# Performance work log

Hardware: AMD Instinct MI355X
Metric: run time of the kernel (lower is better)

## Reference

```python
import jax, jax.numpy as jnp
import numpy as np

ORD = 2  # matches EarthMoverLoss(ord=2)


def _lsa_square(cost):
    """Optimal linear sum assignment (minimize) on a square cost matrix.
    Shortest-augmenting-path algorithm, equivalent to
    scipy.optimize.linear_sum_assignment. Returns col4row: row i -> col4row[i].
    """
    n = cost.shape[0]
    u = np.zeros(n)
    v = np.zeros(n)
    path = np.full(n, -1, dtype=np.int64)
    col4row = np.full(n, -1, dtype=np.int64)
    row4col = np.full(n, -1, dtype=np.int64)
    rows = np.arange(n)
    for cur_row in range(n):
        min_val = 0.0
        i = cur_row
        SR = np.zeros(n, dtype=bool)   # scanned rows
        SC = np.zeros(n, dtype=bool)   # scanned cols
        shortest = np.full(n, np.inf)  # shortest path cost to each col
        sink = -1
        while sink == -1:
            SR[i] = True
            cols = np.flatnonzero(~SC)
            r = min_val + cost[i, cols] - u[i] - v[cols]
            upd = r < shortest[cols]
            cu = cols[upd]
            shortest[cu] = r[upd]
            path[cu] = i
            k = np.argmin(shortest[cols])
            j = cols[k]
            min_val = shortest[j]
            if np.isinf(min_val):
                raise ValueError('infeasible cost matrix')
            SC[j] = True
            if row4col[j] == -1:
                sink = j
            else:
                i = row4col[j]
        # dual variable update
        u[cur_row] += min_val
        others = SR & (rows != cur_row)
        u[others] += min_val - shortest[col4row[others]]
        v[SC] -= min_val - shortest[SC]
        # augment along the alternating path
        j = sink
        while True:
            i = path[j]
            row4col[j] = i
            col4row[i], j = j, col4row[i]
            if i == cur_row:
                break
    return col4row


def _batched_assignment(x, y):
    """Per-sample Euclidean cdist + Hungarian; mirrors the torch module's
    detached CPU/scipy path. Returns [B, N] int permutation of y per sample."""
    xn = np.asarray(jax.device_get(x), dtype=np.float64)
    yn = np.asarray(jax.device_get(y), dtype=np.float64)
    perms = []
    for b in range(xn.shape[0]):
        d2 = ((xn[b, :, None, :] - yn[b, None, :, :]) ** 2).sum(-1)  # [N, N]
        perms.append(_lsa_square(np.sqrt(d2)))
    return jnp.asarray(np.stack(perms))  # [B, N]


def setup_inputs() -> dict:
    key = jax.random.key(0)
    k1, k2 = jax.random.split(key)
    pred = jax.random.normal(k1, (8, 256, 3), dtype=jnp.float32)
    label = jax.random.normal(k2, (8, 256, 3), dtype=jnp.float32)
    return {"pred": pred, "label": label}


def reference(pred, label):
    # Hungarian matching on detached values (scipy returns ind1 = arange for
    # a square cost matrix, so only label is permuted).
    perm = _batched_assignment(pred, label)                      # [B, N]
    matched_y = jnp.take_along_axis(label, perm[:, :, None], axis=1)  # [B, N, D]
    # mean over batch and points of the ord-2 vector norm along coord dim
    return jnp.mean(jnp.linalg.norm(pred - matched_y, ord=ORD, axis=2))
```

## Files before the change

kernel.cpp:

```cpp
#include <hip/hip_runtime.h>
#include <math.h>

#define NPTS 256
#define NB 8

#if __has_builtin(__builtin_amdgcn_sqrtf)
#define FSQRT __builtin_amdgcn_sqrtf
#else
#define FSQRT sqrtf
#endif

__device__ __forceinline__ double dist3d(double ax, double ay, double az,
                                         double bx, double by, double bz) {
#pragma clang fp contract(off)
  double d0 = ax - bx;
  double d1 = ay - by;
  double d2 = az - bz;
  double s = d0 * d0;
  s = s + d1 * d1;
  s = s + d2 * d2;
  return sqrt(s);
}

__device__ __forceinline__ float distf(float ax, float ay, float az,
                                       float bx, float by, float bz) {
  float d0 = ax - bx, d1 = ay - by, d2 = az - bz;
  return FSQRT(d0 * d0 + d1 * d1 + d2 * d2);
}

__device__ __forceinline__ unsigned wave_min_u32(unsigned x) {
  unsigned r = x;
  r = min(r, (unsigned)__builtin_amdgcn_update_dpp((int)r, (int)r, 0x111, 0xF, 0xF, false));
  r = min(r, (unsigned)__builtin_amdgcn_update_dpp((int)r, (int)r, 0x112, 0xF, 0xF, false));
  r = min(r, (unsigned)__builtin_amdgcn_update_dpp((int)r, (int)r, 0x114, 0xF, 0xF, false));
  r = min(r, (unsigned)__builtin_amdgcn_update_dpp((int)r, (int)r, 0x118, 0xF, 0xF, false));
  r = min(r, (unsigned)__builtin_amdgcn_update_dpp((int)r, (int)r, 0x142, 0xF, 0xF, false));
  r = min(r, (unsigned)__builtin_amdgcn_update_dpp((int)r, (int)r, 0x143, 0xF, 0xF, false));
  return (unsigned)__builtin_amdgcn_readlane((int)r, 63);
}

__global__ __launch_bounds__(64) void emd_lsa_kernel(
    const float* __restrict__ pred, const float* __restrict__ label,
    double* __restrict__ partial) {
  __shared__ float4 rowd[NPTS];
  __shared__ float ys0[NPTS], ys1[NPTS], ys2[NPTS];
  __shared__ float short_l[NPTS];
  __shared__ int path_l[NPTS];
  __shared__ int c4r_l[NPTS];
  __shared__ int r4c_l[NPTS];
  __shared__ int sr_l[NPTS];
  __shared__ int bcfr[NPTS];
  __shared__ int fq[NPTS];

  const int lane = threadIdx.x;
  const int b = blockIdx.x;
  const float* xg = pred + (size_t)b * NPTS * 3;
  const float* yg = label + (size_t)b * NPTS * 3;

  const int cid0 = lane * 4, cid1 = cid0 + 1, cid2 = cid0 + 2, cid3 = cid0 + 3;

  float q0x, q0y, q0z, q1x, q1y, q1z, q2x, q2y, q2z, q3x, q3y, q3z;
  float vv0, vv1, vv2, vv3;
  int rc0, rc1, rc2, rc3;

#define INITC(c) { int j = cid##c; \
    rowd[j] = make_float4(xg[j*3+0], xg[j*3+1], xg[j*3+2], 0.0f); \
    float t0 = yg[j*3+0], t1 = yg[j*3+1], t2 = yg[j*3+2]; \
    ys0[j] = t0; ys1[j] = t1; ys2[j] = t2; \
    q##c##x = t0; q##c##y = t1; q##c##z = t2; \
    c4r_l[j] = -1; r4c_l[j] = -1; bcfr[j] = 0x7FFFFFFF; }
  INITC(0) INITC(1) INITC(2) INITC(3)
#undef INITC
  __syncthreads();

  float mm0 = 3.4e38f, mm1 = 3.4e38f, mm2 = 3.4e38f, mm3 = 3.4e38f;
  int im0 = -1, im1 = -1, im2 = -1, im3 = -1;
  for (int i = 0; i < NPTS; ++i) {
    float4 rd = rowd[i];
#define CRED(c) { float d = distf(rd.x, rd.y, rd.z, q##c##x, q##c##y, q##c##z); \
    bool u_ = d < mm##c; mm##c = u_ ? d : mm##c; im##c = u_ ? i : im##c; }
    CRED(0) CRED(1) CRED(2) CRED(3)
#undef CRED
  }
  vv0 = mm0; vv1 = mm1; vv2 = mm2; vv3 = mm3;
  atomicMin(&bcfr[im0], cid0);
  atomicMin(&bcfr[im1], cid1);
  atomicMin(&bcfr[im2], cid2);
  atomicMin(&bcfr[im3], cid3);
  __syncthreads();
  if (bcfr[im0] == cid0) { r4c_l[cid0] = im0; c4r_l[im0] = cid0; }
  if (bcfr[im1] == cid1) { r4c_l[cid1] = im1; c4r_l[im1] = cid1; }
  if (bcfr[im2] == cid2) { r4c_l[cid2] = im2; c4r_l[im2] = cid2; }
  if (bcfr[im3] == cid3) { r4c_l[cid3] = im3; c4r_l[im3] = cid3; }
  __syncthreads();
  rc0 = r4c_l[cid0]; rc1 = r4c_l[cid1]; rc2 = r4c_l[cid2]; rc3 = r4c_l[cid3];

  int nf;
  {
    int4 cc = *(int4*)&c4r_l[cid0];
    bool f0 = cc.x < 0, f1 = cc.y < 0, f2 = cc.z < 0, f3 = cc.w < 0;
    unsigned long long b0 = __ballot(f0), b1 = __ballot(f1);
    unsigned long long b2 = __ballot(f2), b3 = __ballot(f3);
    unsigned long long lt = (1ull << lane) - 1ull;
    int off = __popcll(b0 & lt) + __popcll(b1 & lt) + __popcll(b2 & lt) + __popcll(b3 & lt);
    if (f0) fq[off++] = cid0;
    if (f1) fq[off++] = cid1;
    if (f2) fq[off++] = cid2;
    if (f3) fq[off++] = cid3;
    nf = __popcll(b0) + __popcll(b1) + __popcll(b2) + __popcll(b3);
  }
  __syncthreads();

  const float INF = 3.4e38f;

  for (int t = 0; t < nf; ++t) {
    int cur_row = fq[t];

    float sh0 = INF, sh1 = INF, sh2 = INF, sh3 = INF;
    int pp0 = -1, pp1 = -1, pp2 = -1, pp3 = -1;
    int sc0 = 0, sc1 = 0, sc2 = 0, sc3 = 0;
    *(int4*)&sr_l[cid0] = make_int4(0, 0, 0, 0);
    __syncthreads();

    float min_val = 0.0f;
    int i = cur_row;
    int sink = -1;
    float xi, yi, zi, ui;
    { float4 r0 = rowd[cur_row]; xi = r0.x; yi = r0.y; zi = r0.z; ui = r0.w; }

    while (true) {
      sr_l[i] = 1;
      float base = min_val - ui;
      unsigned k0, k1, k2, k3;
#define SSTEP(c) { float d = distf(xi, yi, zi, q##c##x, q##c##y, q##c##z); \
      float r = (base + d) - vv##c; \
      bool u_ = (r < sh##c) && (sc##c == 0); \
      sh##c = u_ ? r : sh##c; \
      pp##c = u_ ? i : pp##c; \
      unsigned kk = (__float_as_uint(fmaxf(sh##c, 0.0f)) & 0xFFFFFF00u) | (unsigned)cid##c; \
      k##c = sc##c ? 0xFFFFFFFFu : kk; }
      SSTEP(0) SSTEP(1) SSTEP(2) SSTEP(3)
#undef SSTEP
      bool t01 = k1 < k0;
      unsigned ka = t01 ? k1 : k0; int na = t01 ? rc1 : rc0;
      float ea = t01 ? sh1 : sh0;  int pa = t01 ? pp1 : pp0;
      bool t23 = k3 < k2;
      unsigned kb = t23 ? k3 : k2; int nb2 = t23 ? rc3 : rc2;
      float eb = t23 ? sh3 : sh2;  int pb = t23 ? pp3 : pp2;
      bool tf = kb < ka;
      unsigned lkey = tf ? kb : ka; int nl = tf ? nb2 : na;
      float el = tf ? eb : ea;     int pl = tf ? pb : pa;

      float4 pre = rowd[nl < 0 ? 0 : nl];

      unsigned best = wave_min_u32(lkey);
      int jstar = (int)(best & 0xFFu);
      int w = jstar >> 2;

      int nr = __builtin_amdgcn_readlane(nl, w);
      min_val = __int_as_float(__builtin_amdgcn_readlane(__float_as_int(el), w));
      int pj = __builtin_amdgcn_readlane(pl, w);

      short_l[jstar] = min_val;
      path_l[jstar] = pj;
      sc0 |= (cid0 == jstar); sc1 |= (cid1 == jstar);
      sc2 |= (cid2 == jstar); sc3 |= (cid3 == jstar);

      if (nr < 0) { sink = jstar; break; }
      i = nr;
      xi = __int_as_float(__builtin_amdgcn_readlane(__float_as_int(pre.x), w));
      yi = __int_as_float(__builtin_amdgcn_readlane(__float_as_int(pre.y), w));
      zi = __int_as_float(__builtin_amdgcn_readlane(__float_as_int(pre.z), w));
      ui = __int_as_float(__builtin_amdgcn_readlane(__float_as_int(pre.w), w));
    }
    __syncthreads();

#define DUALU(c) { int row = cid##c; \
      if (sr_l[row]) { \
        float du = (row == cur_row) ? min_val : (min_val - short_l[c4r_l[row]]); \
        rowd[row].w += du; } \
      if (sc##c) vv##c -= min_val - sh##c; }
    DUALU(0) DUALU(1) DUALU(2) DUALU(3)
#undef DUALU
    __syncthreads();

    if (lane == 0) {
      int jj = sink;
      while (true) {
        int ii = path_l[jj];
        r4c_l[jj] = ii;
        int tmp = c4r_l[ii];
        c4r_l[ii] = jj;
        jj = tmp;
        if (ii == cur_row) break;
      }
    }
    __syncthreads();
    rc0 = r4c_l[cid0]; rc1 = r4c_l[cid1]; rc2 = r4c_l[cid2]; rc3 = r4c_l[cid3];
    __syncthreads();
  }

  double s = 0.0;
#define FIN(c) { int row = cid##c; int j = c4r_l[row]; float4 rd = rowd[row]; \
    s += dist3d((double)rd.x, (double)rd.y, (double)rd.z, \
                (double)ys0[j], (double)ys1[j], (double)ys2[j]); }
  FIN(0) FIN(1) FIN(2) FIN(3)
#undef FIN
  for (int m = 1; m < 64; m <<= 1) s += __shfl_xor(s, m);
  if (lane == 0) partial[b] = s;
}

__global__ void emd_finalize_kernel(const double* __restrict__ partial,
                                    float* __restrict__ out) {
  if (threadIdx.x == 0 && blockIdx.x == 0) {
    double s = 0.0;
    for (int b = 0; b < NB; ++b) s += partial[b];
    out[0] = (float)(s / (double)(NB * NPTS));
  }
}

extern "C" void kernel_launch(void* const* d_in, const int* in_sizes, int n_in,
                              void* d_out, int out_size, void* d_ws, size_t ws_size,
                              hipStream_t stream) {
  const float* pred = (const float*)d_in[0];
  const float* label = (const float*)d_in[1];
  double* partial = (double*)d_ws;
  emd_lsa_kernel<<<NB, 64, 0, stream>>>(pred, label, partial);
  emd_finalize_kernel<<<1, 64, 0, stream>>>(partial, (float*)d_out);
}
```

Baseline: 1.420 ms.

## Pack two samples per wave and add row-reduction dual initialization

Each 64-lane wave now solves two samples in parallel, one per 32-lane half, with 8 columns per lane. Only 4 blocks are launched instead of 8. A row-reduction pass tightens the dual variables before augmentation, which may shorten the augmenting paths. The per-step cross-lane reduction now uses DPP plus ds_bpermute within each half instead of readlanes, and the wave-wide barriers inside the augment loop are dropped. In exchange each lane does twice the work per step, and both halves run in lockstep until the larger of the two free-row counts is done.

```diff
diff --git a/kernel.cpp b/kernel.cpp
--- a/kernel.cpp
+++ b/kernel.cpp
@@ -10,12 +10,12 @@
 #define FSQRT sqrtf
 #endif
 
+#define REP8(M) M(0) M(1) M(2) M(3) M(4) M(5) M(6) M(7)
+
 __device__ __forceinline__ double dist3d(double ax, double ay, double az,
                                          double bx, double by, double bz) {
 #pragma clang fp contract(off)
-  double d0 = ax - bx;
-  double d1 = ay - by;
-  double d2 = az - bz;
+  double d0 = ax - bx, d1 = ay - by, d2 = az - bz;
   double s = d0 * d0;
   s = s + d1 * d1;
   s = s + d2 * d2;
@@ -28,186 +28,213 @@
   return FSQRT(d0 * d0 + d1 * d1 + d2 * d2);
 }
 
-__device__ __forceinline__ unsigned wave_min_u32(unsigned x) {
+__device__ __forceinline__ unsigned grp_min_bcast(unsigned x, int bad31) {
   unsigned r = x;
   r = min(r, (unsigned)__builtin_amdgcn_update_dpp((int)r, (int)r, 0x111, 0xF, 0xF, false));
   r = min(r, (unsigned)__builtin_amdgcn_update_dpp((int)r, (int)r, 0x112, 0xF, 0xF, false));
   r = min(r, (unsigned)__builtin_amdgcn_update_dpp((int)r, (int)r, 0x114, 0xF, 0xF, false));
   r = min(r, (unsigned)__builtin_amdgcn_update_dpp((int)r, (int)r, 0x118, 0xF, 0xF, false));
   r = min(r, (unsigned)__builtin_amdgcn_update_dpp((int)r, (int)r, 0x142, 0xF, 0xF, false));
-  r = min(r, (unsigned)__builtin_amdgcn_update_dpp((int)r, (int)r, 0x143, 0xF, 0xF, false));
-  return (unsigned)__builtin_amdgcn_readlane((int)r, 63);
-}
+  return (unsigned)__builtin_amdgcn_ds_bpermute(bad31, (int)r);
+}
+
+__device__ __forceinline__ float bperm_f(int ba, float v) {
+  return __int_as_float(__builtin_amdgcn_ds_bpermute(ba, __float_as_int(v)));
+}
+
+#define SEL8(T, res, P, cs) { \
+  T a01 = ((cs) & 1) ? P##1 : P##0; T a23 = ((cs) & 1) ? P##3 : P##2; \
+  T a45 = ((cs) & 1) ? P##5 : P##4; T a67 = ((cs) & 1) ? P##7 : P##6; \
+  T a03 = ((cs) & 2) ? a23 : a01;   T a47 = ((cs) & 2) ? a67 : a45; \
+  res = ((cs) & 4) ? a47 : a03; }
 
 __global__ __launch_bounds__(64) void emd_lsa_kernel(
     const float* __restrict__ pred, const float* __restrict__ label,
     double* __restrict__ partial) {
-  __shared__ float4 rowd[NPTS];
-  __shared__ float ys0[NPTS], ys1[NPTS], ys2[NPTS];
-  __shared__ float short_l[NPTS];
-  __shared__ int path_l[NPTS];
-  __shared__ int c4r_l[NPTS];
-  __shared__ int r4c_l[NPTS];
-  __shared__ int sr_l[NPTS];
-  __shared__ int bcfr[NPTS];
-  __shared__ int fq[NPTS];
+  __shared__ float4 rowd[2 * NPTS];
+  __shared__ float4 colj[2 * NPTS];
+  __shared__ float short_l[2 * NPTS];
+  __shared__ int path_l[2 * NPTS];
+  __shared__ int c4r_l[2 * NPTS];
+  __shared__ int r4c_l[2 * NPTS];
+  __shared__ int sr_l[2 * NPTS];
+  __shared__ int bcfr[2 * NPTS];
+  __shared__ int fq[2 * NPTS];
 
   const int lane = threadIdx.x;
+  const int gid = lane >> 5;
+  const int gl = lane & 31;
+  const int gofs = gid << 8;
   const int b = blockIdx.x;
-  const float* xg = pred + (size_t)b * NPTS * 3;
-  const float* yg = label + (size_t)b * NPTS * 3;
-
-  const int cid0 = lane * 4, cid1 = cid0 + 1, cid2 = cid0 + 2, cid3 = cid0 + 3;
-
-  float q0x, q0y, q0z, q1x, q1y, q1z, q2x, q2y, q2z, q3x, q3y, q3z;
-  float vv0, vv1, vv2, vv3;
-  int rc0, rc1, rc2, rc3;
-
-#define INITC(c) { int j = cid##c; \
-    rowd[j] = make_float4(xg[j*3+0], xg[j*3+1], xg[j*3+2], 0.0f); \
+  const int smp = 2 * b + gid;
+  const float* xg = pred + (size_t)smp * NPTS * 3;
+  const float* yg = label + (size_t)smp * NPTS * 3;
+  const int bad31 = ((lane & 32) | 31) << 2;
+  const int rb = gl << 3;
+
+#define DECL(c) float q##c##x, q##c##y, q##c##z; float vv##c; int rc##c;
+  REP8(DECL)
+#undef DECL
+
+#define INITC(c) { int j = rb + c; int g = gofs + j; \
+    rowd[g] = make_float4(xg[j*3+0], xg[j*3+1], xg[j*3+2], 0.0f); \
     float t0 = yg[j*3+0], t1 = yg[j*3+1], t2 = yg[j*3+2]; \
-    ys0[j] = t0; ys1[j] = t1; ys2[j] = t2; \
+    colj[g] = make_float4(t0, t1, t2, 0.0f); \
     q##c##x = t0; q##c##y = t1; q##c##z = t2; \
-    c4r_l[j] = -1; r4c_l[j] = -1; bcfr[j] = 0x7FFFFFFF; }
-  INITC(0) INITC(1) INITC(2) INITC(3)
+    c4r_l[g] = -1; r4c_l[g] = -1; bcfr[g] = 0x7FFFFFFF; }
+  REP8(INITC)
 #undef INITC
   __syncthreads();
 
-  float mm0 = 3.4e38f, mm1 = 3.4e38f, mm2 = 3.4e38f, mm3 = 3.4e38f;
-  int im0 = -1, im1 = -1, im2 = -1, im3 = -1;
+#define DECLM(c) float mm##c = 3.4e38f; int im##c = -1;
+  REP8(DECLM)
+#undef DECLM
   for (int i = 0; i < NPTS; ++i) {
-    float4 rd = rowd[i];
+    float4 rd = rowd[gofs + i];
 #define CRED(c) { float d = distf(rd.x, rd.y, rd.z, q##c##x, q##c##y, q##c##z); \
     bool u_ = d < mm##c; mm##c = u_ ? d : mm##c; im##c = u_ ? i : im##c; }
-    CRED(0) CRED(1) CRED(2) CRED(3)
+    REP8(CRED)
 #undef CRED
   }
-  vv0 = mm0; vv1 = mm1; vv2 = mm2; vv3 = mm3;
-  atomicMin(&bcfr[im0], cid0);
-  atomicMin(&bcfr[im1], cid1);
-  atomicMin(&bcfr[im2], cid2);
-  atomicMin(&bcfr[im3], cid3);
-  __syncthreads();
-  if (bcfr[im0] == cid0) { r4c_l[cid0] = im0; c4r_l[im0] = cid0; }
-  if (bcfr[im1] == cid1) { r4c_l[cid1] = im1; c4r_l[im1] = cid1; }
-  if (bcfr[im2] == cid2) { r4c_l[cid2] = im2; c4r_l[im2] = cid2; }
-  if (bcfr[im3] == cid3) { r4c_l[cid3] = im3; c4r_l[im3] = cid3; }
-  __syncthreads();
-  rc0 = r4c_l[cid0]; rc1 = r4c_l[cid1]; rc2 = r4c_l[cid2]; rc3 = r4c_l[cid3];
+#define WRV(c) colj[gofs + rb + c].w = mm##c; atomicMin(&bcfr[gofs + im##c], rb + c);
+  REP8(WRV)
+#undef WRV
+  __syncthreads();
+#define GRD(c) if (bcfr[gofs + im##c] == rb + c) { r4c_l[gofs + rb + c] = im##c; c4r_l[gofs + im##c] = rb + c; }
+  REP8(GRD)
+#undef GRD
+  __syncthreads();
+
+  {
+#define LDR(c) float4 rD##c = rowd[gofs + rb + c]; int ja##c = c4r_l[gofs + rb + c]; float mu##c = 3.4e38f;
+    REP8(LDR)
+#undef LDR
+    for (int j = 0; j < NPTS; ++j) {
+      float4 cj = colj[gofs + j];
+#define RT(c) { float d = distf(rD##c.x, rD##c.y, rD##c.z, cj.x, cj.y, cj.z) - cj.w; \
+      d = (j == ja##c) ? 3.4e38f : d; mu##c = fminf(mu##c, d); }
+      REP8(RT)
+#undef RT
+    }
+#define WRT(c) if (ja##c >= 0) { colj[gofs + ja##c].w -= mu##c; rowd[gofs + rb + c].w = mu##c; }
+    REP8(WRT)
+#undef WRT
+  }
+  __syncthreads();
+#define LDV(c) vv##c = colj[gofs + rb + c].w; rc##c = r4c_l[gofs + rb + c];
+  REP8(LDV)
+#undef LDV
 
   int nf;
   {
-    int4 cc = *(int4*)&c4r_l[cid0];
-    bool f0 = cc.x < 0, f1 = cc.y < 0, f2 = cc.z < 0, f3 = cc.w < 0;
-    unsigned long long b0 = __ballot(f0), b1 = __ballot(f1);
-    unsigned long long b2 = __ballot(f2), b3 = __ballot(f3);
-    unsigned long long lt = (1ull << lane) - 1ull;
-    int off = __popcll(b0 & lt) + __popcll(b1 & lt) + __popcll(b2 & lt) + __popcll(b3 & lt);
-    if (f0) fq[off++] = cid0;
-    if (f1) fq[off++] = cid1;
-    if (f2) fq[off++] = cid2;
-    if (f3) fq[off++] = cid3;
-    nf = __popcll(b0) + __popcll(b1) + __popcll(b2) + __popcll(b3);
-  }
-  __syncthreads();
+#define FLG(c) int fl##c = (c4r_l[gofs + rb + c] < 0) ? 1 : 0; \
+    unsigned long long bb##c = __ballot(fl##c); \
+    unsigned gm##c = (unsigned)(bb##c >> (gid * 32));
+    REP8(FLG)
+#undef FLG
+    unsigned lt = (1u << gl) - 1u;
+    int off = __popc(gm0 & lt) + __popc(gm1 & lt) + __popc(gm2 & lt) + __popc(gm3 & lt)
+            + __popc(gm4 & lt) + __popc(gm5 & lt) + __popc(gm6 & lt) + __popc(gm7 & lt);
+#define PUT(c) if (fl##c) { fq[gofs + off] = rb + c; off++; }
+    REP8(PUT)
+#undef PUT
+    nf = __popc(gm0) + __popc(gm1) + __popc(gm2) + __popc(gm3)
+       + __popc(gm4) + __popc(gm5) + __popc(gm6) + __popc(gm7);
+  }
+  __syncthreads();
+  int onf = __shfl(nf, lane ^ 32);
+  int nfmax = max(nf, onf);
 
   const float INF = 3.4e38f;
 
-  for (int t = 0; t < nf; ++t) {
-    int cur_row = fq[t];
-
-    float sh0 = INF, sh1 = INF, sh2 = INF, sh3 = INF;
-    int pp0 = -1, pp1 = -1, pp2 = -1, pp3 = -1;
-    int sc0 = 0, sc1 = 0, sc2 = 0, sc3 = 0;
-    *(int4*)&sr_l[cid0] = make_int4(0, 0, 0, 0);
-    __syncthreads();
-
-    float min_val = 0.0f;
-    int i = cur_row;
-    int sink = -1;
-    float xi, yi, zi, ui;
-    { float4 r0 = rowd[cur_row]; xi = r0.x; yi = r0.y; zi = r0.z; ui = r0.w; }
-
-    while (true) {
-      sr_l[i] = 1;
-      float base = min_val - ui;
-      unsigned k0, k1, k2, k3;
-#define SSTEP(c) { float d = distf(xi, yi, zi, q##c##x, q##c##y, q##c##z); \
-      float r = (base + d) - vv##c; \
-      bool u_ = (r < sh##c) && (sc##c == 0); \
-      sh##c = u_ ? r : sh##c; \
-      pp##c = u_ ? i : pp##c; \
-      unsigned kk = (__float_as_uint(fmaxf(sh##c, 0.0f)) & 0xFFFFFF00u) | (unsigned)cid##c; \
-      k##c = sc##c ? 0xFFFFFFFFu : kk; }
-      SSTEP(0) SSTEP(1) SSTEP(2) SSTEP(3)
+  for (int t = 0; t < nfmax; ++t) {
+    bool act = (t < nf);
+    if (act) {
+      int cur_row = fq[gofs + t];
+#define SINI(c) float sh##c = INF; int pp##c = -1;
+      REP8(SINI)
+#undef SINI
+      int scm = 0;
+      *(int4*)&sr_l[gofs + rb] = make_int4(0, 0, 0, 0);
+      *(int4*)&sr_l[gofs + rb + 4] = make_int4(0, 0, 0, 0);
+      float4 r0 = rowd[gofs + cur_row];
+      float xi = r0.x, yi = r0.y, zi = r0.z, ui = r0.w;
+      float min_val = 0.0f;
+      int i = cur_row;
+      int sink = -1;
+
+      while (true) {
+        sr_l[gofs + i] = 1;
+        float base_ = min_val - ui;
+#define SSTEP(c) unsigned k##c; { float d = distf(xi, yi, zi, q##c##x, q##c##y, q##c##z); \
+        float r = (base_ + d) - vv##c; \
+        int scb = (scm >> c) & 1; \
+        bool u_ = (r < sh##c) && !scb; \
+        sh##c = u_ ? r : sh##c; pp##c = u_ ? i : pp##c; \
+        unsigned kk = (__float_as_uint(fmaxf(sh##c, 0.0f)) & 0xFFFFFF00u) | (unsigned)(rb + c); \
+        k##c = scb ? 0xFFFFFFFFu : kk; }
+        REP8(SSTEP)
 #undef SSTEP
-      bool t01 = k1 < k0;
-      unsigned ka = t01 ? k1 : k0; int na = t01 ? rc1 : rc0;
-      float ea = t01 ? sh1 : sh0;  int pa = t01 ? pp1 : pp0;
-      bool t23 = k3 < k2;
-      unsigned kb = t23 ? k3 : k2; int nb2 = t23 ? rc3 : rc2;
-      float eb = t23 ? sh3 : sh2;  int pb = t23 ? pp3 : pp2;
-      bool tf = kb < ka;
-      unsigned lkey = tf ? kb : ka; int nl = tf ? nb2 : na;
-      float el = tf ? eb : ea;     int pl = tf ? pb : pa;
-
-      float4 pre = rowd[nl < 0 ? 0 : nl];
-
-      unsigned best = wave_min_u32(lkey);
-      int jstar = (int)(best & 0xFFu);
-      int w = jstar >> 2;
-
-      int nr = __builtin_amdgcn_readlane(nl, w);
-      min_val = __int_as_float(__builtin_amdgcn_readlane(__float_as_int(el), w));
-      int pj = __builtin_amdgcn_readlane(pl, w);
-
-      short_l[jstar] = min_val;
-      path_l[jstar] = pj;
-      sc0 |= (cid0 == jstar); sc1 |= (cid1 == jstar);
-      sc2 |= (cid2 == jstar); sc3 |= (cid3 == jstar);
-
-      if (nr < 0) { sink = jstar; break; }
-      i = nr;
-      xi = __int_as_float(__builtin_amdgcn_readlane(__float_as_int(pre.x), w));
-      yi = __int_as_float(__builtin_amdgcn_readlane(__float_as_int(pre.y), w));
-      zi = __int_as_float(__builtin_amdgcn_readlane(__float_as_int(pre.z), w));
-      ui = __int_as_float(__builtin_amdgcn_readlane(__float_as_int(pre.w), w));
+        unsigned lkey = min(min(min(k0, k1), min(k2, k3)),
+                            min(min(k4, k5), min(k6, k7)));
+        unsigned best = grp_min_bcast(lkey, bad31);
+        int jstar = (int)(best & 0xFFu);
+        int csel = jstar & 7;
+        int wlane = (lane & 32) | (jstar >> 3);
+
+        float els; SEL8(float, els, sh, csel)
+        int nls;   SEL8(int, nls, rc, csel)
+        int pps;   SEL8(int, pps, pp, csel)
+        if (lane == wlane) {
+          short_l[gofs + jstar] = els;
+          path_l[gofs + jstar] = pps;
+        }
+        scm |= ((gl == (jstar >> 3)) ? 1 : 0) << csel;
+
+        int ba = wlane << 2;
+        min_val = bperm_f(ba, els);
+        int nr = __builtin_amdgcn_ds_bpermute(ba, nls);
+        if (nr < 0) { sink = jstar; break; }
+        i = nr;
+        float4 ri = rowd[gofs + i];
+        xi = ri.x; yi = ri.y; zi = ri.z; ui = ri.w;
+      }
+
+#define DUALU(c) { int row = rb + c; \
+      if (sr_l[gofs + row]) { \
+        float du = (row == cur_row) ? min_val : (min_val - short_l[gofs + c4r_l[gofs + row]]); \
+        rowd[gofs + row].w += du; } \
+      if ((scm >> c) & 1) vv##c -= min_val - sh##c; }
+      REP8(DUALU)
+#undef DUALU
+
+      if (gl == 0) {
+        int jj = sink;
+        while (true) {
+          int ii = path_l[gofs + jj];
+          r4c_l[gofs + jj] = ii;
+          int tmp = c4r_l[gofs + ii];
+          c4r_l[gofs + ii] = jj;
+          jj = tmp;
+          if (ii == cur_row) break;
+        }
+      }
+#define RFR(c) rc##c = r4c_l[gofs + rb + c];
+      REP8(RFR)
+#undef RFR
     }
-    __syncthreads();
-
-#define DUALU(c) { int row = cid##c; \
-      if (sr_l[row]) { \
-        float du = (row == cur_row) ? min_val : (min_val - short_l[c4r_l[row]]); \
-        rowd[row].w += du; } \
-      if (sc##c) vv##c -= min_val - sh##c; }
-    DUALU(0) DUALU(1) DUALU(2) DUALU(3)
-#undef DUALU
-    __syncthreads();
-
-    if (lane == 0) {
-      int jj = sink;
-      while (true) {
-        int ii = path_l[jj];
-        r4c_l[jj] = ii;
-        int tmp = c4r_l[ii];
-        c4r_l[ii] = jj;
-        jj = tmp;
-        if (ii == cur_row) break;
-      }
-    }
-    __syncthreads();
-    rc0 = r4c_l[cid0]; rc1 = r4c_l[cid1]; rc2 = r4c_l[cid2]; rc3 = r4c_l[cid3];
-    __syncthreads();
-  }
+  }
+  __syncthreads();
 
   double s = 0.0;
-#define FIN(c) { int row = cid##c; int j = c4r_l[row]; float4 rd = rowd[row]; \
+#define FIN(c) { int row = rb + c; int j = c4r_l[gofs + row]; \
+    float4 rd = rowd[gofs + row]; float4 cj = colj[gofs + j]; \
     s += dist3d((double)rd.x, (double)rd.y, (double)rd.z, \
-                (double)ys0[j], (double)ys1[j], (double)ys2[j]); }
-  FIN(0) FIN(1) FIN(2) FIN(3)
+                (double)cj.x, (double)cj.y, (double)cj.z); }
+  REP8(FIN)
 #undef FIN
-  for (int m = 1; m < 64; m <<= 1) s += __shfl_xor(s, m);
-  if (lane == 0) partial[b] = s;
+  for (int m = 1; m < 32; m <<= 1) s += __shfl_xor(s, m);
+  if (gl == 0) partial[smp] = s;
 }
 
 __global__ void emd_finalize_kernel(const double* __restrict__ partial,
@@ -225,6 +252,6 @@
   const float* pred = (const float*)d_in[0];
   const float* label = (const float*)d_in[1];
   double* partial = (double*)d_ws;
-  emd_lsa_kernel<<<NB, 64, 0, stream>>>(pred, label, partial);
+  emd_lsa_kernel<<<4, 64, 0, stream>>>(pred, label, partial);
   emd_finalize_kernel<<<1, 64, 0, stream>>>(partial, (float*)d_out);
 }
```

Result: slower. 2.782 ms (+96.0%).
